# Optimization experiments

Hardware: AMD Instinct MI355X
Metric: run time of the kernel (lower is better)

Reference implementation:

```python
import jax, jax.numpy as jnp
import numpy as np

N_NODES = 100000
N_EDGES = 1600000
IN_CH = 128
HID = 128
OUT = 128


def gcn_conv(x, src, dst, dinv, W, b, n_nodes):
    """GCNConv with self-loops already folded into (src, dst, dinv).
    out[v] = sum_{(u->v)} dinv[u]*dinv[v] * (x @ W)[u] + b
    """
    xw = x @ W                                   # [N, F_out]
    norm = dinv[src] * dinv[dst]                 # [E+N]
    msg = xw[src] * norm[:, None]                # [E+N, F_out] (gather)
    out = jax.ops.segment_sum(msg, dst, num_segments=n_nodes)  # scatter-add
    return out + b


def setup_inputs() -> dict:
    key = jax.random.key(0)
    k = jax.random.split(key, 8)
    x = jax.random.normal(k[0], (N_NODES, IN_CH), dtype=jnp.float32)
    edge_index = jax.random.randint(k[1], (2, N_EDGES), 0, N_NODES, dtype=jnp.int64)
    s = 0.05
    W1 = jax.random.normal(k[2], (IN_CH, HID), dtype=jnp.float32) * s
    b1 = jnp.zeros((HID,), dtype=jnp.float32)
    W2 = jax.random.normal(k[3], (HID, HID), dtype=jnp.float32) * s
    b2 = jnp.zeros((HID,), dtype=jnp.float32)
    Wfc = jax.random.normal(k[4], (HID, OUT), dtype=jnp.float32) * s
    bfc = jnp.zeros((OUT,), dtype=jnp.float32)
    return {"x": x, "edge_index": edge_index, "W1": W1, "b1": b1,
            "W2": W2, "b2": b2, "Wfc": Wfc, "bfc": bfc}


def reference(x, edge_index, W1, b1, W2, b2, Wfc, bfc):
    n = x.shape[0]
    loop = jnp.arange(n, dtype=edge_index.dtype)
    src = jnp.concatenate([edge_index[0], loop])   # add self loops (PyG default)
    dst = jnp.concatenate([edge_index[1], loop])
    # symmetric normalization: deg over targets incl. self loops
    deg = jax.ops.segment_sum(jnp.ones_like(dst, dtype=x.dtype), dst, num_segments=n)
    dinv = jnp.where(deg > 0, jax.lax.rsqrt(deg), 0.0)
    h = jax.nn.relu(gcn_conv(x, src, dst, dinv, W1, b1, n))
    h = jax.nn.relu(gcn_conv(h, src, dst, dinv, W2, b2, n))
    pooled = jnp.mean(h, axis=0, keepdims=True)    # [1, HID]
    return pooled @ Wfc + bfc                      # [1, OUT]
```

## Files before the change

### kernel.cpp

```cpp
#include <hip/hip_runtime.h>
#include <stdint.h>

typedef unsigned short ushort_t;
typedef __attribute__((ext_vector_type(8))) short bf16x8;
typedef __attribute__((ext_vector_type(4))) float f32x4;
typedef __attribute__((ext_vector_type(2))) float f32x2;

#define BKT_SHIFT 7
#define BKT_W     128
#define NB_MAX    1024
#define KB_THREADS 1024
#define KB_EPT    4
#define KB_CHUNK  (KB_THREADS * KB_EPT)
#define BCAP      2560
#define CSTRIDE   2944
#define PSLICES   8


__device__ __forceinline__ ushort_t f2bf(float f) {
    union { float f; uint32_t u; } a; a.f = f;
    uint32_t u = a.u;
    uint32_t r = (u + 0x7FFFu + ((u >> 16) & 1u)) >> 16;
    return (ushort_t)r;
}
__device__ __forceinline__ float bf_lo(uint32_t p) { return __uint_as_float(p << 16); }
__device__ __forceinline__ float bf_hi(uint32_t p) { return __uint_as_float(p & 0xFFFF0000u); }

__global__ __launch_bounds__(256) void kW_init(const float* __restrict__ W1,
                                               const float* __restrict__ W2,
                                               ushort_t* __restrict__ Wt1,
                                               ushort_t* __restrict__ Wt2,
                                               int* __restrict__ bcnt,
                                               float* __restrict__ pooled,
                                               int* __restrict__ counter,
                                               uint8_t* __restrict__ xwq, int n) {
    int b = blockIdx.x, t = threadIdx.x;
    if (b < 64) {
        int i = b * 256 + t;
        int k = i >> 7, nn = i & 127;
        Wt1[nn * 128 + k] = f2bf(W1[i]);
        Wt2[nn * 128 + k] = f2bf(W2[i]);
    } else {
        for (int i = t; i < NB_MAX; i += 256) bcnt[i] = 0;
        for (int i = t; i < PSLICES * 128; i += 256) pooled[i] = 0.f;
        if (t < 32) ((uint32_t*)(xwq + (size_t)n * 128))[t] = 0u;
        if (t == 0) *counter = 0;
    }
}

__global__ __launch_bounds__(KB_THREADS) void kB_bucket(const int* __restrict__ src,
                                                        const int* __restrict__ dst, int E, int NB,
                                                        int* __restrict__ bcnt,
                                                        uint32_t* __restrict__ bpack) {
    __shared__ int lh[NB_MAX];
    const int t = threadIdx.x;
    for (int i = t; i < NB; i += KB_THREADS) lh[i] = 0;
    __syncthreads();

    const int base = blockIdx.x * KB_CHUNK + t * KB_EPT;
    int d[KB_EPT], rank[KB_EPT];
    const bool full = (base + KB_EPT - 1 < E);
    if (full) {
        int4 dv = *(const int4*)(dst + base);
        d[0] = dv.x; d[1] = dv.y; d[2] = dv.z; d[3] = dv.w;
#pragma unroll
        for (int i = 0; i < KB_EPT; i++)
            rank[i] = atomicAdd(&lh[d[i] >> BKT_SHIFT], 1);
    } else {
#pragma unroll
        for (int i = 0; i < KB_EPT; i++) {
            int e = base + i;
            if (e < E) {
                d[i] = dst[e];
                rank[i] = atomicAdd(&lh[d[i] >> BKT_SHIFT], 1);
            } else {
                d[i] = -1; rank[i] = 0;
            }
        }
    }
    __syncthreads();
    for (int i = t; i < NB; i += KB_THREADS) {
        int c = lh[i];
        lh[i] = c ? atomicAdd(&bcnt[i], c) : 0;
    }
    __syncthreads();
    if (full) {
        int4 sv = *(const int4*)(src + base);
        int s[KB_EPT] = {sv.x, sv.y, sv.z, sv.w};
#pragma unroll
        for (int i = 0; i < KB_EPT; i++) {
            int bkt = d[i] >> BKT_SHIFT;
            size_t pos = (size_t)bkt * BCAP + lh[bkt] + rank[i];
            bpack[pos] = ((uint32_t)s[i] << BKT_SHIFT) | (uint32_t)(d[i] & (BKT_W - 1));
        }
    } else {
#pragma unroll
        for (int i = 0; i < KB_EPT; i++) {
            if (d[i] >= 0) {
                int bkt = d[i] >> BKT_SHIFT;
                size_t pos = (size_t)bkt * BCAP + lh[bkt] + rank[i];
                bpack[pos] = ((uint32_t)src[base + i] << BKT_SHIFT) | (uint32_t)(d[i] & (BKT_W - 1));
            }
        }
    }
}

__global__ __launch_bounds__(256) void kC_csr(const uint32_t* __restrict__ bpack,
                                              const int* __restrict__ bcnt, int NB, int n,
                                              float* __restrict__ dinv,
                                              int* __restrict__ offs,
                                              int* __restrict__ ends,
                                              int* __restrict__ csr) {
    __shared__ int pr[BKT_W];
    __shared__ int cnt[BKT_W];
    __shared__ int cur[BKT_W];
    __shared__ int pend[BKT_W];

    const int t = threadIdx.x;
    const int b = blockIdx.x;
    const int nb0 = b << BKT_SHIFT;
    const int wlen = min(BKT_W, n - nb0);
    const int cntb = bcnt[b];
    const uint32_t* bp = bpack + (size_t)b * BCAP;
    const int base = b * CSTRIDE;

    if (t < BKT_W) cnt[t] = 0;
    __syncthreads();
    for (int e = t; e < cntb; e += 256)
        atomicAdd(&cnt[bp[e] & (BKT_W - 1)], 1);
    __syncthreads();

    int v = (t < BKT_W) ? cnt[t] : 0;
    int pv = (v + 3) & ~3;
    if (t < BKT_W) pr[t] = pv;
    __syncthreads();
    for (int off = 1; off < BKT_W; off <<= 1) {
        int x = (t >= off && t < BKT_W) ? pr[t - off] : 0;
        __syncthreads();
        if (t < BKT_W) pr[t] += x;
        __syncthreads();
    }
    if (t < BKT_W) {
        int st = base + pr[t] - pv;
        cur[t] = st;
        pend[t] = st + pv;
        if (t < wlen) {
            offs[nb0 + t] = st;
            ends[nb0 + t] = st + pv;
            dinv[nb0 + t] = rsqrtf((float)(v + 1));
        }
    }
    __syncthreads();

    for (int e = t; e < cntb; e += 256) {
        uint32_t p = bp[e];
        int pos = atomicAdd(&cur[p & (BKT_W - 1)], 1);
        csr[pos] = (int)(p >> BKT_SHIFT);
    }
    __syncthreads();
    if (t < BKT_W) {
        int qe = pend[t];
        for (int q = cur[t]; q < qe; q++) csr[q] = n;
    }
}

__global__ __launch_bounds__(256) void k_gemm1(const float* __restrict__ x,
                                               const ushort_t* __restrict__ Wt,
                                               const float* __restrict__ dinv,
                                               uint8_t* __restrict__ C, int n) {
    __shared__ ushort_t al[64 * 136];
    __shared__ ushort_t wl[128 * 136];
    const int t = threadIdx.x;
    const int l = t & 63;
    const int wave = t >> 6;
    const int lane15 = l & 15;
    const int quad = l >> 4;
    const int m0 = blockIdx.x * 64;
    const int rows = min(64, n - m0);

#pragma unroll
    for (int i = 0; i < 8; i++) {
        int f = t + 256 * i;
        int r = f >> 4, c = f & 15;
        *(uint4*)(&wl[r * 136 + c * 8]) = ((const uint4*)Wt)[f];
    }
    {
        const float4* Ap = (const float4*)(x + (size_t)m0 * 128);
        int nf = rows * 32;
#pragma unroll
        for (int i = 0; i < 8; i++) {
            int f = t + 256 * i;
            float4 vv = make_float4(0.f, 0.f, 0.f, 0.f);
            if (f < nf) vv = Ap[f];
            ushort4 us;
            us.x = f2bf(vv.x); us.y = f2bf(vv.y); us.z = f2bf(vv.z); us.w = f2bf(vv.w);
            int r = f >> 5, c = f & 31;
            *(ushort4*)(&al[r * 136 + c * 4]) = us;
        }
    }
    __syncthreads();

    f32x4 acc[8];
#pragma unroll
    for (int nt = 0; nt < 8; nt++) acc[nt] = (f32x4){0.f, 0.f, 0.f, 0.f};

    const int arow = wave * 16 + lane15;
#pragma unroll
    for (int kt = 0; kt < 4; kt++) {
        bf16x8 af = *(const bf16x8*)(&al[arow * 136 + kt * 32 + quad * 8]);
#pragma unroll
        for (int nt = 0; nt < 8; nt++) {
            bf16x8 bfr = *(const bf16x8*)(&wl[(nt * 16 + lane15) * 136 + kt * 32 + quad * 8]);
            acc[nt] = __builtin_amdgcn_mfma_f32_16x16x32_bf16(af, bfr, acc[nt], 0, 0, 0);
        }
    }

    const int rbase = m0 + wave * 16 + quad * 4;
    float dsc[4];
#pragma unroll
    for (int r = 0; r < 4; r++)
        dsc[r] = (rbase + r < n) ? dinv[rbase + r] : 0.f;
#pragma unroll
    for (int nt = 0; nt < 8; nt++) {
        int c0 = nt * 16 + lane15;
#pragma unroll
        for (int r = 0; r < 4; r += 2) {
            int pk = __builtin_amdgcn_cvt_pk_fp8_f32(acc[nt][r] * dsc[r],
                                                     acc[nt][r + 1] * dsc[r + 1], 0, false);
            int row0 = rbase + r, row1 = rbase + r + 1;
            if (row0 < n) C[(size_t)row0 * 128 + c0] = (uint8_t)pk;
            if (row1 < n) C[(size_t)row1 * 128 + c0] = (uint8_t)(pk >> 8);
        }
    }
}

__global__ __launch_bounds__(256) void k_gemm_mfma(const ushort_t* __restrict__ A,
                                                   const ushort_t* __restrict__ Wt,
                                                   const float* __restrict__ dinv,
                                                   uint8_t* __restrict__ C, int n) {
    __shared__ ushort_t al[64 * 136];
    __shared__ ushort_t wl[128 * 136];
    const int t = threadIdx.x;
    const int l = t & 63;
    const int wave = t >> 6;
    const int lane15 = l & 15;
    const int quad = l >> 4;
    const int m0 = blockIdx.x * 64;
    const int rows = min(64, n - m0);

#pragma unroll
    for (int i = 0; i < 8; i++) {
        int f = t + 256 * i;
        int r = f >> 4, c = f & 15;
        *(uint4*)(&wl[r * 136 + c * 8]) = ((const uint4*)Wt)[f];
    }
    {
        const uint4* Ap = (const uint4*)(A + (size_t)m0 * 128);
        int nf = rows * 16;
#pragma unroll
        for (int i = 0; i < 4; i++) {
            int f = t + 256 * i;
            uint4 v = make_uint4(0, 0, 0, 0);
            if (f < nf) v = Ap[f];
            int r = f >> 4, c = f & 15;
            *(uint4*)(&al[r * 136 + c * 8]) = v;
        }
    }
    __syncthreads();

    f32x4 acc[8];
#pragma unroll
    for (int nt = 0; nt < 8; nt++) acc[nt] = (f32x4){0.f, 0.f, 0.f, 0.f};

    const int arow = wave * 16 + lane15;
#pragma unroll
    for (int kt = 0; kt < 4; kt++) {
        bf16x8 af = *(const bf16x8*)(&al[arow * 136 + kt * 32 + quad * 8]);
#pragma unroll
        for (int nt = 0; nt < 8; nt++) {
            bf16x8 bfr = *(const bf16x8*)(&wl[(nt * 16 + lane15) * 136 + kt * 32 + quad * 8]);
            acc[nt] = __builtin_amdgcn_mfma_f32_16x16x32_bf16(af, bfr, acc[nt], 0, 0, 0);
        }
    }

    const int rbase = m0 + wave * 16 + quad * 4;
    float dsc[4];
#pragma unroll
    for (int r = 0; r < 4; r++)
        dsc[r] = (rbase + r < n) ? dinv[rbase + r] : 0.f;
#pragma unroll
    for (int nt = 0; nt < 8; nt++) {
        int c0 = nt * 16 + lane15;
#pragma unroll
        for (int r = 0; r < 4; r += 2) {
            int pk = __builtin_amdgcn_cvt_pk_fp8_f32(acc[nt][r] * dsc[r],
                                                     acc[nt][r + 1] * dsc[r + 1], 0, false);
            int row0 = rbase + r, row1 = rbase + r + 1;
            if (row0 < n) C[(size_t)row0 * 128 + c0] = (uint8_t)pk;
            if (row1 < n) C[(size_t)row1 * 128 + c0] = (uint8_t)(pk >> 8);
        }
    }
}

__global__ __launch_bounds__(256) void k_agg(const ushort_t* __restrict__ xw,
                                             const int* __restrict__ offsets,
                                             const int* __restrict__ ends,
                                             const int* __restrict__ csr,
                                             const float* __restrict__ dinv,
                                             const float* __restrict__ bias,
                                             ushort_t* __restrict__ out, int n) {
    const int l = threadIdx.x & 63;
    const int wave = (blockIdx.x << 2) | (threadIdx.x >> 6);
    const int wstride = gridDim.x << 2;
    const float2 bb = ((const float2*)bias)[l];
    uint32_t* out32 = (uint32_t*)out;

    for (int v = wave; v < n; v += wstride) {
        uint32_t pv = (uint32_t)xw[(size_t)v * 64 + l];
        f32x2 fs = __builtin_amdgcn_cvt_pk_f32_fp8((int)pv, false);
        float ax = fs.x, ay = fs.y;

        int e  = __builtin_amdgcn_readfirstlane(offsets[v]);
        int e1 = __builtin_amdgcn_readfirstlane(ends[v]);

        for (; e + 15 < e1; e += 16) {
            const int4* c4 = (const int4*)(csr + e);
            int4 w0 = c4[0], w1 = c4[1], w2 = c4[2], w3 = c4[3];
            int u[16];
            u[0]  = __builtin_amdgcn_readfirstlane(w0.x);
            u[1]  = __builtin_amdgcn_readfirstlane(w0.y);
            u[2]  = __builtin_amdgcn_readfirstlane(w0.z);
            u[3]  = __builtin_amdgcn_readfirstlane(w0.w);
            u[4]  = __builtin_amdgcn_readfirstlane(w1.x);
            u[5]  = __builtin_amdgcn_readfirstlane(w1.y);
            u[6]  = __builtin_amdgcn_readfirstlane(w1.z);
            u[7]  = __builtin_amdgcn_readfirstlane(w1.w);
            u[8]  = __builtin_amdgcn_readfirstlane(w2.x);
            u[9]  = __builtin_amdgcn_readfirstlane(w2.y);
            u[10] = __builtin_amdgcn_readfirstlane(w2.z);
            u[11] = __builtin_amdgcn_readfirstlane(w2.w);
            u[12] = __builtin_amdgcn_readfirstlane(w3.x);
            u[13] = __builtin_amdgcn_readfirstlane(w3.y);
            u[14] = __builtin_amdgcn_readfirstlane(w3.z);
            u[15] = __builtin_amdgcn_readfirstlane(w3.w);
            uint32_t p[16];
#pragma unroll
            for (int i = 0; i < 16; i++) p[i] = (uint32_t)xw[(size_t)u[i] * 64 + l];
#pragma unroll
            for (int i = 0; i < 16; i++) {
                f32x2 f = __builtin_amdgcn_cvt_pk_f32_fp8((int)p[i], false);
                ax += f.x; ay += f.y;
            }
        }
        for (; e + 7 < e1; e += 8) {
            const int4* c4 = (const int4*)(csr + e);
            int4 w0 = c4[0], w1 = c4[1];
            int u[8];
            u[0] = __builtin_amdgcn_readfirstlane(w0.x);
            u[1] = __builtin_amdgcn_readfirstlane(w0.y);
            u[2] = __builtin_amdgcn_readfirstlane(w0.z);
            u[3] = __builtin_amdgcn_readfirstlane(w0.w);
            u[4] = __builtin_amdgcn_readfirstlane(w1.x);
            u[5] = __builtin_amdgcn_readfirstlane(w1.y);
            u[6] = __builtin_amdgcn_readfirstlane(w1.z);
            u[7] = __builtin_amdgcn_readfirstlane(w1.w);
            uint32_t p[8];
#pragma unroll
            for (int i = 0; i < 8; i++) p[i] = (uint32_t)xw[(size_t)u[i] * 64 + l];
#pragma unroll
            for (int i = 0; i < 8; i++) {
                f32x2 f = __builtin_amdgcn_cvt_pk_f32_fp8((int)p[i], false);
                ax += f.x; ay += f.y;
            }
        }
        for (; e + 3 < e1; e += 4) {
            int4 w0 = *(const int4*)(csr + e);
            int u[4];
            u[0] = __builtin_amdgcn_readfirstlane(w0.x);
            u[1] = __builtin_amdgcn_readfirstlane(w0.y);
            u[2] = __builtin_amdgcn_readfirstlane(w0.z);
            u[3] = __builtin_amdgcn_readfirstlane(w0.w);
            uint32_t p[4];
#pragma unroll
            for (int i = 0; i < 4; i++) p[i] = (uint32_t)xw[(size_t)u[i] * 64 + l];
#pragma unroll
            for (int i = 0; i < 4; i++) {
                f32x2 f = __builtin_amdgcn_cvt_pk_f32_fp8((int)p[i], false);
                ax += f.x; ay += f.y;
            }
        }

        float dv = dinv[v];
        float ox = fmaxf(fmaf(ax, dv, bb.x), 0.f);
        float oy = fmaxf(fmaf(ay, dv, bb.y), 0.f);
        out32[(size_t)v * 64 + l] = ((uint32_t)f2bf(oy) << 16) | (uint32_t)f2bf(ox);
    }
}

__global__ __launch_bounds__(256) void k_poolfc(const ushort_t* __restrict__ h,
                                                float* __restrict__ pooled, int n,
                                                const float* __restrict__ Wfc,
                                                const float* __restrict__ bfc,
                                                float* __restrict__ out, float invN,
                                                int* __restrict__ counter) {
    __shared__ float red[512];
    __shared__ int lastFlag;
    __shared__ float pl[128];
    const int t = threadIdx.x;
    const int l = t & 63;
    const int wv = (blockIdx.x << 2) | (t >> 6);
    const int ws = gridDim.x << 2;
    const uint32_t* h32 = (const uint32_t*)h;

    const int span = (n + ws - 1) / ws;
    int r0 = wv * span;
    int r1 = min(n, r0 + span);
    float sx = 0.f, sy = 0.f;
    int r = r0;
    for (; r + 3 < r1; r += 4) {
        uint32_t p0 = h32[(size_t)r * 64 + l];
        uint32_t p1 = h32[(size_t)(r + 1) * 64 + l];
        uint32_t p2 = h32[(size_t)(r + 2) * 64 + l];
        uint32_t p3 = h32[(size_t)(r + 3) * 64 + l];
        sx += bf_lo(p0) + bf_lo(p1) + bf_lo(p2) + bf_lo(p3);
        sy += bf_hi(p0) + bf_hi(p1) + bf_hi(p2) + bf_hi(p3);
    }
    for (; r < r1; r++) {
        uint32_t p = h32[(size_t)r * 64 + l];
        sx += bf_lo(p); sy += bf_hi(p);
    }
    red[t] = sx;
    red[256 + t] = sy;
    __syncthreads();
    float* slice = pooled + (blockIdx.x & (PSLICES - 1)) * 128;
    if (t < 64) {
        sx = red[t] + red[t + 64] + red[t + 128] + red[t + 192];
        sy = red[256 + t] + red[256 + t + 64] + red[256 + t + 128] + red[256 + t + 192];
        atomicAdd(&slice[2 * l], sx);
        atomicAdd(&slice[2 * l + 1], sy);
    }
    __threadfence();
    __syncthreads();
    if (t == 0) {
        int old = atomicAdd(counter, 1);
        lastFlag = (old == (int)gridDim.x - 1);
    }
    __syncthreads();
    if (lastFlag) {
        if (t < 128) {
            float acc = 0.f;
#pragma unroll
            for (int s = 0; s < PSLICES; s++)
                acc += atomicAdd(&pooled[s * 128 + t], 0.f);
            pl[t] = acc;
        }
        __syncthreads();
        if (t < 128) {
            float acc = bfc[t];
#pragma unroll 8
            for (int k = 0; k < 128; k++)
                acc = fmaf(pl[k] * invN, Wfc[k * 128 + t], acc);
            out[t] = acc;
        }
    }
}

extern "C" void kernel_launch(void* const* d_in, const int* in_sizes, int n_in,
                              void* d_out, int out_size, void* d_ws, size_t ws_size,
                              hipStream_t stream) {
    const float* x    = (const float*)d_in[0];
    const int*   ei   = (const int*)d_in[1];
    const float* W1   = (const float*)d_in[2];
    const float* b1   = (const float*)d_in[3];
    const float* W2   = (const float*)d_in[4];
    const float* b2   = (const float*)d_in[5];
    const float* Wfc  = (const float*)d_in[6];
    const float* bfc  = (const float*)d_in[7];
    float*       out  = (float*)d_out;

    const int n = in_sizes[0] / 128;
    const int E = in_sizes[1] / 2;
    const int* src = ei;
    const int* dst = ei + E;
    const int NB = (n + BKT_W - 1) >> BKT_SHIFT;

    char* w = (char*)d_ws;
    uint8_t*  xwq = (uint8_t*)w;  w += (size_t)(n + 1) * 128;
    ushort_t* h   = (ushort_t*)w; w += (size_t)n * 128 * sizeof(ushort_t);
    int*      csr = (int*)w;      w += (size_t)NB * CSTRIDE * sizeof(int);
    uint32_t* bpack = (uint32_t*)w; w += (size_t)NB * BCAP * sizeof(uint32_t);
    float* dinv = (float*)w;  w += (size_t)n * sizeof(float);
    int*   offs = (int*)w;    w += (size_t)n * sizeof(int);
    int*   ends = (int*)w;    w += (size_t)n * sizeof(int);
    w = (char*)(((uintptr_t)w + 127) & ~(uintptr_t)127);
    int*   bcnt  = (int*)w;   w += NB_MAX * sizeof(int);
    int*   counter = (int*)w; w += 32 * sizeof(int);
    float* pooled = (float*)w; w += PSLICES * 128 * sizeof(float);
    ushort_t* Wt1 = (ushort_t*)w; w += 16384 * sizeof(ushort_t);
    ushort_t* Wt2 = (ushort_t*)w; w += 16384 * sizeof(ushort_t);

    const int ntiles64 = (n + 63) / 64;
    const float invN = 1.0f / (float)n;

    kW_init<<<65, 256, 0, stream>>>(W1, W2, Wt1, Wt2, bcnt, pooled, counter, xwq, n);
    kB_bucket<<<(E + KB_CHUNK - 1) / KB_CHUNK, KB_THREADS, 0, stream>>>(src, dst, E, NB, bcnt, bpack);
    kC_csr<<<NB, 256, 0, stream>>>(bpack, bcnt, NB, n, dinv, offs, ends, csr);
    k_gemm1<<<ntiles64, 256, 0, stream>>>(x, Wt1, dinv, xwq, n);

    k_agg<<<8192, 256, 0, stream>>>((const ushort_t*)xwq, offs, ends, csr, dinv, b1, h, n);
    k_gemm_mfma<<<ntiles64, 256, 0, stream>>>(h, Wt2, dinv, xwq, n);
    k_agg<<<8192, 256, 0, stream>>>((const ushort_t*)xwq, offs, ends, csr, dinv, b2, h, n);

    k_poolfc<<<256, 256, 0, stream>>>(h, pooled, n, Wfc, bfc, out, invN, counter);
}
```

Baseline: 268.9 us.

## Fuse mean-pooling into second aggregation and split out tiny FC kernel

The second aggregation kernel now accumulates the per-node ReLU outputs into per-thread sums and reduces them into sliced pooled buffers with atomics, instead of writing the bf16 hidden matrix. A separate single-block FC kernel reads the slices and applies Wfc. This removes the write and re-read of the full N x 128 hidden tensor and the last-block counter logic, but adds an extra small launch and atomics at the end of each of the 8192 blocks. The CSR-build kernel block size also grows from 256 to 512 threads.

Result: no change. 270.4 us (+0.5%).

```diff
diff --git a/kernel.cpp b/kernel.cpp
--- a/kernel.cpp
+++ b/kernel.cpp
@@ -14,6 +14,7 @@
 #define KB_CHUNK  (KB_THREADS * KB_EPT)
 #define BCAP      2560
 #define CSTRIDE   2944
+#define CSR_THREADS 512
 #define PSLICES   8
 
 
@@ -105,12 +106,12 @@
     }
 }
 
-__global__ __launch_bounds__(256) void kC_csr(const uint32_t* __restrict__ bpack,
-                                              const int* __restrict__ bcnt, int NB, int n,
-                                              float* __restrict__ dinv,
-                                              int* __restrict__ offs,
-                                              int* __restrict__ ends,
-                                              int* __restrict__ csr) {
+__global__ __launch_bounds__(CSR_THREADS) void kC_csr(const uint32_t* __restrict__ bpack,
+                                                      const int* __restrict__ bcnt, int NB, int n,
+                                                      float* __restrict__ dinv,
+                                                      int* __restrict__ offs,
+                                                      int* __restrict__ ends,
+                                                      int* __restrict__ csr) {
     __shared__ int pr[BKT_W];
     __shared__ int cnt[BKT_W];
     __shared__ int cur[BKT_W];
@@ -126,7 +127,7 @@
 
     if (t < BKT_W) cnt[t] = 0;
     __syncthreads();
-    for (int e = t; e < cntb; e += 256)
+    for (int e = t; e < cntb; e += CSR_THREADS)
         atomicAdd(&cnt[bp[e] & (BKT_W - 1)], 1);
     __syncthreads();
 
@@ -152,7 +153,7 @@
     }
     __syncthreads();
 
-    for (int e = t; e < cntb; e += 256) {
+    for (int e = t; e < cntb; e += CSR_THREADS) {
         uint32_t p = bp[e];
         int pos = atomicAdd(&cur[p & (BKT_W - 1)], 1);
         csr[pos] = (int)(p >> BKT_SHIFT);
@@ -308,12 +309,15 @@
                                              const int* __restrict__ csr,
                                              const float* __restrict__ dinv,
                                              const float* __restrict__ bias,
-                                             ushort_t* __restrict__ out, int n) {
+                                             ushort_t* __restrict__ out, int n,
+                                             float* __restrict__ pooled) {
+    __shared__ float red[512];
     const int l = threadIdx.x & 63;
     const int wave = (blockIdx.x << 2) | (threadIdx.x >> 6);
     const int wstride = gridDim.x << 2;
     const float2 bb = ((const float2*)bias)[l];
     uint32_t* out32 = (uint32_t*)out;
+    float psx = 0.f, psy = 0.f;
 
     for (int v = wave; v < n; v += wstride) {
         uint32_t pv = (uint32_t)xw[(size_t)v * 64 + l];
@@ -393,76 +397,43 @@
         float dv = dinv[v];
         float ox = fmaxf(fmaf(ax, dv, bb.x), 0.f);
         float oy = fmaxf(fmaf(ay, dv, bb.y), 0.f);
-        out32[(size_t)v * 64 + l] = ((uint32_t)f2bf(oy) << 16) | (uint32_t)f2bf(ox);
-    }
-}
-
-__global__ __launch_bounds__(256) void k_poolfc(const ushort_t* __restrict__ h,
-                                                float* __restrict__ pooled, int n,
-                                                const float* __restrict__ Wfc,
-                                                const float* __restrict__ bfc,
-                                                float* __restrict__ out, float invN,
-                                                int* __restrict__ counter) {
-    __shared__ float red[512];
-    __shared__ int lastFlag;
+        if (pooled == nullptr) {
+            out32[(size_t)v * 64 + l] = ((uint32_t)f2bf(oy) << 16) | (uint32_t)f2bf(ox);
+        } else {
+            psx += ox; psy += oy;
+        }
+    }
+
+    if (pooled != nullptr) {
+        const int t = threadIdx.x;
+        red[t] = psx;
+        red[256 + t] = psy;
+        __syncthreads();
+        if (t < 64) {
+            float sx = red[t] + red[t + 64] + red[t + 128] + red[t + 192];
+            float sy = red[256 + t] + red[256 + t + 64] + red[256 + t + 128] + red[256 + t + 192];
+            float* slice = pooled + (blockIdx.x & (PSLICES - 1)) * 128;
+            atomicAdd(&slice[2 * t], sx);
+            atomicAdd(&slice[2 * t + 1], sy);
+        }
+    }
+}
+
+__global__ __launch_bounds__(128) void k_fc(const float* __restrict__ pooled,
+                                            const float* __restrict__ Wfc,
+                                            const float* __restrict__ bfc,
+                                            float* __restrict__ out, float invN) {
     __shared__ float pl[128];
     const int t = threadIdx.x;
-    const int l = t & 63;
-    const int wv = (blockIdx.x << 2) | (t >> 6);
-    const int ws = gridDim.x << 2;
-    const uint32_t* h32 = (const uint32_t*)h;
-
-    const int span = (n + ws - 1) / ws;
-    int r0 = wv * span;
-    int r1 = min(n, r0 + span);
-    float sx = 0.f, sy = 0.f;
-    int r = r0;
-    for (; r + 3 < r1; r += 4) {
-        uint32_t p0 = h32[(size_t)r * 64 + l];
-        uint32_t p1 = h32[(size_t)(r + 1) * 64 + l];
-        uint32_t p2 = h32[(size_t)(r + 2) * 64 + l];
-        uint32_t p3 = h32[(size_t)(r + 3) * 64 + l];
-        sx += bf_lo(p0) + bf_lo(p1) + bf_lo(p2) + bf_lo(p3);
-        sy += bf_hi(p0) + bf_hi(p1) + bf_hi(p2) + bf_hi(p3);
-    }
-    for (; r < r1; r++) {
-        uint32_t p = h32[(size_t)r * 64 + l];
-        sx += bf_lo(p); sy += bf_hi(p);
-    }
-    red[t] = sx;
-    red[256 + t] = sy;
-    __syncthreads();
-    float* slice = pooled + (blockIdx.x & (PSLICES - 1)) * 128;
-    if (t < 64) {
-        sx = red[t] + red[t + 64] + red[t + 128] + red[t + 192];
-        sy = red[256 + t] + red[256 + t + 64] + red[256 + t + 128] + red[256 + t + 192];
-        atomicAdd(&slice[2 * l], sx);
-        atomicAdd(&slice[2 * l + 1], sy);
-    }
-    __threadfence();
-    __syncthreads();
-    if (t == 0) {
-        int old = atomicAdd(counter, 1);
-        lastFlag = (old == (int)gridDim.x - 1);
-    }
-    __syncthreads();
-    if (lastFlag) {
-        if (t < 128) {
-            float acc = 0.f;
-#pragma unroll
-            for (int s = 0; s < PSLICES; s++)
-                acc += atomicAdd(&pooled[s * 128 + t], 0.f);
-            pl[t] = acc;
-        }
-        __syncthreads();
-        if (t < 128) {
-            float acc = bfc[t];
+    float acc = 0.f;
+#pragma unroll
+    for (int s = 0; s < PSLICES; s++) acc += pooled[s * 128 + t];
+    pl[t] = acc * invN;
+    __syncthreads();
+    float o = bfc[t];
 #pragma unroll 8
-            for (int k = 0; k < 128; k++)
-                acc = fmaf(pl[k] * invN, Wfc[k * 128 + t], acc);
-            out[t] = acc;
-        }
-    }
+    for (int k = 0; k < 128; k++) o = fmaf(pl[k], Wfc[k * 128 + t], o);
+    out[t] = o;
 }
 
 extern "C" void kernel_launch(void* const* d_in, const int* in_sizes, int n_in,
@@ -504,12 +475,12 @@
 
     kW_init<<<65, 256, 0, stream>>>(W1, W2, Wt1, Wt2, bcnt, pooled, counter, xwq, n);
     kB_bucket<<<(E + KB_CHUNK - 1) / KB_CHUNK, KB_THREADS, 0, stream>>>(src, dst, E, NB, bcnt, bpack);
-    kC_csr<<<NB, 256, 0, stream>>>(bpack, bcnt, NB, n, dinv, offs, ends, csr);
+    kC_csr<<<NB, CSR_THREADS, 0, stream>>>(bpack, bcnt, NB, n, dinv, offs, ends, csr);
     k_gemm1<<<ntiles64, 256, 0, stream>>>(x, Wt1, dinv, xwq, n);
 
-    k_agg<<<8192, 256, 0, stream>>>((const ushort_t*)xwq, offs, ends, csr, dinv, b1, h, n);
+    k_agg<<<8192, 256, 0, stream>>>((const ushort_t*)xwq, offs, ends, csr, dinv, b1, h, n, nullptr);
     k_gemm_mfma<<<ntiles64, 256, 0, stream>>>(h, Wt2, dinv, xwq, n);
-    k_agg<<<8192, 256, 0, stream>>>((const ushort_t*)xwq, offs, ends, csr, dinv, b2, h, n);
-
-    k_poolfc<<<256, 256, 0, stream>>>(h, pooled, n, Wfc, bfc, out, invN, counter);
-}
+    k_agg<<<8192, 256, 0, stream>>>((const ushort_t*)xwq, offs, ends, csr, dinv, b2, h, n, pooled);
+
+    k_fc<<<1, 128, 0, stream>>>(pooled, Wfc, bfc, out, invN);
+}
```
